# Kernel optimization log

Measured on AMD Instinct MI355X. Metric: run time of the kernel, lower is better.

Reference implementation:

```python
import jax, jax.numpy as jnp
import numpy as np

H = 16  # n_heads


def setup_inputs() -> dict:
    key = jax.random.key(0)
    ks = jax.random.split(key, 8)
    N, L, dm = 4, 2048, 1024
    scale = 0.02
    rn = lambda k, shape: jax.random.normal(k, shape, dtype=jnp.float32)
    return {
        "queries": rn(ks[0], (N, L, dm)),
        "keys": rn(ks[1], (N, L, dm)),
        "values": rn(ks[2], (N, L, dm)),
        "Wq": rn(ks[3], (dm, dm)) * scale, "bq": jnp.zeros((dm,), jnp.float32),
        "Wk": rn(ks[4], (dm, dm)) * scale, "bk": jnp.zeros((dm,), jnp.float32),
        "Wv": rn(ks[5], (dm, dm)) * scale, "bv": jnp.zeros((dm,), jnp.float32),
        "Wo": rn(ks[6], (dm, dm)) * scale, "bo": jnp.zeros((dm,), jnp.float32),
    }


def _forward(queries, keys, values, Wq, bq, Wk, bk, Wv, bv, Wo, bo):
    N, L, _ = queries.shape
    q = (queries @ Wq + bq).reshape(N, L, H, -1)  # [N,L,H,D]
    k = (keys @ Wk + bk).reshape(N, L, H, -1)     # [N,L,H,D]
    v = (values @ Wv + bv).reshape(N, L, H, -1)   # [N,L,H,K]
    qp = jax.nn.elu(q) + 1.0
    kp = jax.nn.elu(k) + 1.0
    D = qp.shape[-1]
    K = v.shape[-1]

    # Causal linear attention: cumulative outer-product recurrence over time.
    def step(sums, inp):
        q_t, k_t, v_t = inp  # each [N,H,D] / [N,H,K]
        sums = sums + jnp.einsum('bhd,bhk->bhdk', k_t, v_t)
        out_t = jnp.einsum('bhdk,bhd->bhk', sums, q_t)
        return sums, out_t

    init = jnp.zeros((N, H, D, K), qp.dtype)
    xs = (jnp.swapaxes(qp, 0, 1), jnp.swapaxes(kp, 0, 1), jnp.swapaxes(v, 0, 1))
    _, res = jax.lax.scan(step, init, xs)  # [L,N,H,K]
    res = jnp.swapaxes(res, 0, 1)          # [N,L,H,K]
    # Original divides elementwise by cumsum of query features (D == K).
    Z = jnp.cumsum(qp, axis=1)             # [N,L,H,D]
    out = (res / Z).reshape(N, L, -1)
    return out @ Wo + bo


def reference(queries, keys, values, Wq, bq, Wk, bk, Wv, bv, Wo, bo):
    return _forward(queries, keys, values, Wq, bq, Wk, bk, Wv, bv, Wo, bo)
```

## Files before the change

kernel.cpp:

```cpp
#include <hip/hip_runtime.h>
#include <hip/hip_bf16.h>

typedef __hip_bfloat16 bf16;

#define N_B   4
#define LSEQ  2048
#define DM    1024
#define NH    16
#define HD    64
#define MROWS (N_B * LSEQ)
#define TCH   64
#define NC    (LSEQ / TCH)
#define PS    72

typedef short bf16x8 __attribute__((ext_vector_type(8)));
typedef float f32x4  __attribute__((ext_vector_type(4)));

__device__ __forceinline__ float u2f(unsigned short u){ return __uint_as_float(((unsigned)u) << 16); }
__device__ __forceinline__ unsigned short f2u(float x){
    bf16 h = __float2bfloat16(x);
    return *reinterpret_cast<unsigned short*>(&h);
}

__device__ __forceinline__ void g2l16(const void* g, void* l) {
    __builtin_amdgcn_global_load_lds(
        (const __attribute__((address_space(1))) unsigned int*)g,
        (__attribute__((address_space(3))) unsigned int*)l, 16, 0, 0);
}

__global__ __launch_bounds__(256) void cvt3_f32_bf16(
    const float* __restrict__ x0, const float* __restrict__ x1, const float* __restrict__ x2,
    bf16* __restrict__ y0, bf16* __restrict__ y1, bf16* __restrict__ y2, int per)
{
    int which = blockIdx.x / per;
    const float* x = (which == 0) ? x0 : (which == 1) ? x1 : x2;
    bf16* y = (which == 0) ? y0 : (which == 1) ? y1 : y2;
    int i = (blockIdx.x - which * per) * 256 + threadIdx.x;
    float4 v = ((const float4*)x)[i];
    ushort4 o = make_ushort4(f2u(v.x), f2u(v.y), f2u(v.z), f2u(v.w));
    ((ushort4*)y)[i] = o;
}

__global__ __launch_bounds__(256) void transpose_w4(
    const float* __restrict__ W0, const float* __restrict__ W1,
    const float* __restrict__ W2, const float* __restrict__ W3,
    bf16* __restrict__ T0, bf16* __restrict__ T1,
    bf16* __restrict__ T2, bf16* __restrict__ T3)
{
    const int z = blockIdx.z;
    const float* W = (z == 0) ? W0 : (z == 1) ? W1 : (z == 2) ? W2 : W3;
    bf16* Wt = (z == 0) ? T0 : (z == 1) ? T1 : (z == 2) ? T2 : T3;

    __shared__ unsigned short t[64][65];
    const int n0 = blockIdx.x * 64;
    const int k0 = blockIdx.y * 64;
    #pragma unroll
    for (int i = 0; i < 16; ++i) {
        int e = i * 256 + threadIdx.x;
        int r = e >> 6, c = e & 63;
        t[c][r] = f2u(W[(size_t)(k0 + r) * DM + n0 + c]);
    }
    __syncthreads();
    #pragma unroll
    for (int i = 0; i < 16; ++i) {
        int e = i * 256 + threadIdx.x;
        int r = e >> 6, c = e & 63;
        ((unsigned short*)Wt)[(size_t)(n0 + r) * DM + k0 + c] = t[r][c];
    }
}

template <typename TO>
__global__ __launch_bounds__(256) void gemm_mfma3(
    const bf16* __restrict__ A0, const bf16* __restrict__ A1, const bf16* __restrict__ A2,
    const bf16* __restrict__ B0, const bf16* __restrict__ B1, const bf16* __restrict__ B2,
    const float* __restrict__ c0, const float* __restrict__ c1, const float* __restrict__ c2,
    TO* __restrict__ C0, TO* __restrict__ C1, TO* __restrict__ C2,
    int actMask, int M, int N, int K)
{
    const int z = blockIdx.z;
    const bf16* A  = (z == 0) ? A0 : (z == 1) ? A1 : A2;
    const bf16* Bt = (z == 0) ? B0 : (z == 1) ? B1 : B2;
    const float* bias = (z == 0) ? c0 : (z == 1) ? c1 : c2;
    TO* C = (z == 0) ? C0 : (z == 1) ? C1 : C2;
    const int act = (actMask >> z) & 1;

    __shared__ __align__(16) short As[128 * 32];
    __shared__ __align__(16) short Bs[128 * 32];

    const int tid  = threadIdx.x;
    const int m0   = blockIdx.x * 128;
    const int n0   = blockIdx.y * 128;
    const int wave = tid >> 6;
    const int lane = tid & 63;
    const int wm   = (wave >> 1) * 64;
    const int wn   = (wave & 1) * 64;
    const int quad = lane >> 4;
    const int l16  = lane & 15;
    const int ksw  = (quad ^ (l16 & 3)) * 8;

    f32x4 acc[4][4] = {};

    for (int k0i = 0; k0i < K; k0i += 32) {
        #pragma unroll
        for (int i = 0; i < 2; ++i) {
            int e = i * 256 + tid;
            int row = e >> 2, kg = e & 3;
            int kgs = (kg ^ (row & 3)) * 8;
            g2l16(A  + (size_t)(m0 + row) * K + k0i + kgs, As + e * 8);
            g2l16(Bt + (size_t)(n0 + row) * K + k0i + kgs, Bs + e * 8);
        }
        __syncthreads();

        bf16x8 af[4], bf_[4];
        #pragma unroll
        for (int mi = 0; mi < 4; ++mi)
            af[mi] = *(const bf16x8*)&As[(wm + mi * 16 + l16) * 32 + ksw];
        #pragma unroll
        for (int ni = 0; ni < 4; ++ni)
            bf_[ni] = *(const bf16x8*)&Bs[(wn + ni * 16 + l16) * 32 + ksw];

        #pragma unroll
        for (int mi = 0; mi < 4; ++mi)
            #pragma unroll
            for (int ni = 0; ni < 4; ++ni)
                acc[mi][ni] = __builtin_amdgcn_mfma_f32_16x16x32_bf16(
                    af[mi], bf_[ni], acc[mi][ni], 0, 0, 0);

        __syncthreads();
    }

    #pragma unroll
    for (int ni = 0; ni < 4; ++ni) {
        int col = n0 + wn + ni * 16 + l16;
        float bv = bias[col];
        #pragma unroll
        for (int mi = 0; mi < 4; ++mi) {
            #pragma unroll
            for (int r = 0; r < 4; ++r) {
                int row = m0 + wm + mi * 16 + quad * 4 + r;
                float x = acc[mi][ni][r] + bv;
                if (act) x = (x > 0.f) ? (x + 1.f) : __expf(x);
                if constexpr (sizeof(TO) == 2)
                    ((bf16*)C)[(size_t)row * N + col] = __float2bfloat16(x);
                else
                    ((float*)C)[(size_t)row * N + col] = x;
            }
        }
    }
}

__global__ __launch_bounds__(256) void chunk_state(
    const bf16* __restrict__ qp, const bf16* __restrict__ kp,
    const bf16* __restrict__ v,
    bf16* __restrict__ chunkSB, float* __restrict__ chunkZ)
{
    __shared__ __align__(16) unsigned short kpT_s[64 * PS];
    __shared__ __align__(16) unsigned short vT_s [64 * PS];
    __shared__ __align__(16) unsigned short qp_s [64 * PS];
    __shared__ float red[4][64];

    const int bh = blockIdx.x;
    const int c  = blockIdx.y;
    const int n  = bh >> 4, h = bh & 15;
    const int tid = threadIdx.x;
    const size_t rowbase = (size_t)n * LSEQ + (size_t)c * TCH;

    #pragma unroll
    for (int r = 0; r < 4; ++r) {
        int q = r * 256 + tid;
        int t = q >> 4, c0 = (q & 15) * 4;
        size_t g = (rowbase + t) * DM + h * HD + c0;
        ushort4 ku = *(const ushort4*)((const unsigned short*)kp + g);
        ushort4 vu = *(const ushort4*)((const unsigned short*)v  + g);
        ushort4 qu = *(const ushort4*)((const unsigned short*)qp + g);
        kpT_s[(c0+0)*PS + t] = ku.x;  kpT_s[(c0+1)*PS + t] = ku.y;
        kpT_s[(c0+2)*PS + t] = ku.z;  kpT_s[(c0+3)*PS + t] = ku.w;
        vT_s [(c0+0)*PS + t] = vu.x;  vT_s [(c0+1)*PS + t] = vu.y;
        vT_s [(c0+2)*PS + t] = vu.z;  vT_s [(c0+3)*PS + t] = vu.w;
        *(ushort4*)&qp_s[t * PS + c0] = qu;
    }
    __syncthreads();

    const int wave = tid >> 6, lane = tid & 63;
    const int quad = lane >> 4, l16 = lane & 15;

    f32x4 acc[4] = {};
    #pragma unroll
    for (int kk = 0; kk < 2; ++kk) {
        bf16x8 af = *(const bf16x8*)&kpT_s[(wave*16 + l16) * PS + kk*32 + quad*8];
        #pragma unroll
        for (int ni = 0; ni < 4; ++ni) {
            bf16x8 bfr = *(const bf16x8*)&vT_s[(ni*16 + l16) * PS + kk*32 + quad*8];
            acc[ni] = __builtin_amdgcn_mfma_f32_16x16x32_bf16(af, bfr, acc[ni], 0, 0, 0);
        }
    }
    unsigned short* Sout = (unsigned short*)chunkSB + (((size_t)bh * NC + c) << 12);
    #pragma unroll
    for (int ni = 0; ni < 4; ++ni) {
        int k = ni*16 + l16;
        #pragma unroll
        for (int r = 0; r < 4; ++r) {
            int d = wave*16 + quad*4 + r;
            Sout[d * 64 + k] = f2u(acc[ni][r]);
        }
    }

    {
        int d = tid & 63, part = tid >> 6;
        float s = 0.f;
        #pragma unroll
        for (int t = part*16; t < part*16 + 16; ++t)
            s += u2f(qp_s[t * PS + d]);
        red[part][d] = s;
    }
    __syncthreads();
    if (tid < 64)
        chunkZ[((size_t)bh * NC + c) * 64 + tid] =
            red[0][tid] + red[1][tid] + red[2][tid] + red[3][tid];
}

__global__ __launch_bounds__(256) void prefix_state(
    const bf16* __restrict__ chunkSB, bf16* __restrict__ SpB,
    float* __restrict__ chunkZ)
{
    const int bh = blockIdx.x;
    const int elem = blockIdx.y * 256 + threadIdx.x;
    const unsigned short* p = (const unsigned short*)chunkSB + (((size_t)bh * NC) << 12) + elem;
    unsigned short* o = (unsigned short*)SpB + (((size_t)bh * NC) << 12) + elem;
    float run = 0.f;
    #pragma unroll
    for (int c = 0; c < NC; ++c) {
        float x = u2f(p[(size_t)c << 12]);
        o[(size_t)c << 12] = f2u(run);
        run += x;
    }
    if (blockIdx.y == 0 && threadIdx.x < 64) {
        float* pz = chunkZ + (size_t)bh * NC * 64 + threadIdx.x;
        float rz = 0.f;
        for (int c = 0; c < NC; ++c) {
            float x = pz[c * 64];
            pz[c * 64] = rz;
            rz += x;
        }
    }
}

__global__ __launch_bounds__(256) void chunk_attn(
    const bf16* __restrict__ qp, const bf16* __restrict__ kp,
    const bf16* __restrict__ v, const bf16* __restrict__ SpB,
    const float* __restrict__ chunkZ, bf16* __restrict__ att)
{
    __shared__ __align__(16) unsigned short qp_s [64 * PS];
    __shared__ __align__(16) unsigned short kp_s [64 * PS];
    __shared__ __align__(16) unsigned short SpT_s[64 * PS];
    __shared__ __align__(16) unsigned short vT_s [64 * PS];
    __shared__ __align__(16) unsigned short qpT_s[64 * PS];
    __shared__ __align__(16) unsigned short P_s  [64 * PS];

    const int bh = blockIdx.x;
    const int c  = blockIdx.y;
    const int n  = bh >> 4, h = bh & 15;
    const int tid = threadIdx.x;
    const size_t rowbase = (size_t)n * LSEQ + (size_t)c * TCH;
    const unsigned short* Spb = (const unsigned short*)SpB + (((size_t)bh * NC + c) << 12);

    #pragma unroll
    for (int r = 0; r < 4; ++r) {
        int q = r * 256 + tid;
        int t = q >> 4, c0 = (q & 15) * 4;
        size_t g = (rowbase + t) * DM + h * HD + c0;
        ushort4 qu = *(const ushort4*)((const unsigned short*)qp + g);
        ushort4 ku = *(const ushort4*)((const unsigned short*)kp + g);
        ushort4 vu = *(const ushort4*)((const unsigned short*)v  + g);
        ushort4 su = *(const ushort4*)(Spb + q * 4);
        *(ushort4*)&qp_s[t * PS + c0] = qu;
        *(ushort4*)&kp_s[t * PS + c0] = ku;
        vT_s [(c0+0)*PS + t] = vu.x;  vT_s [(c0+1)*PS + t] = vu.y;
        vT_s [(c0+2)*PS + t] = vu.z;  vT_s [(c0+3)*PS + t] = vu.w;
        qpT_s[(c0+0)*PS + t] = qu.x;  qpT_s[(c0+1)*PS + t] = qu.y;
        qpT_s[(c0+2)*PS + t] = qu.z;  qpT_s[(c0+3)*PS + t] = qu.w;
        SpT_s[(c0+0)*PS + t] = su.x;  SpT_s[(c0+1)*PS + t] = su.y;
        SpT_s[(c0+2)*PS + t] = su.z;  SpT_s[(c0+3)*PS + t] = su.w;
    }
    __syncthreads();

    const int wave = tid >> 6, lane = tid & 63;
    const int quad = lane >> 4, l16 = lane & 15;
    const int mrow = wave * 16;

    f32x4 acc[4]  = {};
    f32x4 zacc[4] = {};
    f32x4 pacc[4] = {};

    const unsigned short ONE = 0x3F80;

    #pragma unroll
    for (int kk = 0; kk < 2; ++kk) {
        bf16x8 af = *(const bf16x8*)&qp_s[(mrow + l16) * PS + kk*32 + quad*8];
        bf16x8 tf;
        #pragma unroll
        for (int j = 0; j < 8; ++j) {
            int s = kk*32 + quad*8 + j;
            tf[j] = (short)((s <= mrow + l16) ? ONE : 0);
        }
        #pragma unroll
        for (int ni = 0; ni < 4; ++ni) {
            int boff = (ni*16 + l16) * PS + kk*32 + quad*8;
            bf16x8 b_sp = *(const bf16x8*)&SpT_s[boff];
            bf16x8 b_kp = *(const bf16x8*)&kp_s [boff];
            bf16x8 b_qt = *(const bf16x8*)&qpT_s[boff];
            acc [ni] = __builtin_amdgcn_mfma_f32_16x16x32_bf16(af, b_sp, acc [ni], 0, 0, 0);
            pacc[ni] = __builtin_amdgcn_mfma_f32_16x16x32_bf16(af, b_kp, pacc[ni], 0, 0, 0);
            zacc[ni] = __builtin_amdgcn_mfma_f32_16x16x32_bf16(tf, b_qt, zacc[ni], 0, 0, 0);
        }
    }

    #pragma unroll
    for (int ni = 0; ni < 4; ++ni) {
        int s = ni*16 + l16;
        #pragma unroll
        for (int r = 0; r < 4; ++r) {
            int t = mrow + quad*4 + r;
            float pv = (s <= t) ? pacc[ni][r] : 0.f;
            P_s[t * PS + s] = f2u(pv);
        }
    }
    __syncthreads();

    #pragma unroll
    for (int kk = 0; kk < 2; ++kk) {
        bf16x8 af = *(const bf16x8*)&P_s[(mrow + l16) * PS + kk*32 + quad*8];
        #pragma unroll
        for (int ni = 0; ni < 4; ++ni) {
            bf16x8 b_v = *(const bf16x8*)&vT_s[(ni*16 + l16) * PS + kk*32 + quad*8];
            acc[ni] = __builtin_amdgcn_mfma_f32_16x16x32_bf16(af, b_v, acc[ni], 0, 0, 0);
        }
    }

    #pragma unroll
    for (int ni = 0; ni < 4; ++ni) {
        int k = ni*16 + l16;
        float zp = chunkZ[((size_t)bh * NC + c) * 64 + k];
        #pragma unroll
        for (int r = 0; r < 4; ++r) {
            int t = mrow + quad*4 + r;
            float o = acc[ni][r] / (zp + zacc[ni][r]);
            ((unsigned short*)att)[(rowbase + t) * DM + h * HD + k] = f2u(o);
        }
    }
}

extern "C" void kernel_launch(void* const* d_in, const int* in_sizes, int n_in,
                              void* d_out, int out_size, void* d_ws, size_t ws_size,
                              hipStream_t stream)
{
    const float* queries = (const float*)d_in[0];
    const float* keys    = (const float*)d_in[1];
    const float* values  = (const float*)d_in[2];
    const float* Wq = (const float*)d_in[3];
    const float* bq = (const float*)d_in[4];
    const float* Wk = (const float*)d_in[5];
    const float* bk = (const float*)d_in[6];
    const float* Wv = (const float*)d_in[7];
    const float* bv = (const float*)d_in[8];
    const float* Wo = (const float*)d_in[9];
    const float* bo = (const float*)d_in[10];
    float* out = (float*)d_out;

    char* w = (char*)d_ws;
    const size_t E2 = (size_t)MROWS * DM * 2;
    const size_t WB = (size_t)DM * DM * 2;
    bf16* qb  = (bf16*)(w + 0 * E2);
    bf16* kb  = (bf16*)(w + 1 * E2);
    bf16* vb  = (bf16*)(w + 2 * E2);
    bf16* Wqt = (bf16*)(w + 3 * E2 + 0 * WB);
    bf16* Wkt = (bf16*)(w + 3 * E2 + 1 * WB);
    bf16* Wvt = (bf16*)(w + 3 * E2 + 2 * WB);
    bf16* Wot = (bf16*)(w + 3 * E2 + 3 * WB);
    bf16* qp  = (bf16*)(w + 3 * E2 + 4 * WB);
    bf16* kp  = (bf16*)(w + 4 * E2 + 4 * WB);
    bf16* vv  = (bf16*)(w + 5 * E2 + 4 * WB);
    bf16* SpB = (bf16*)(w + 6 * E2 + 4 * WB);
    bf16*  chunkSB = kb;
    float* chunkZ  = (float*)Wqt;
    bf16*  att     = qb;

    const int n4 = (MROWS * DM) / 4;
    const int per = n4 / 256;
    cvt3_f32_bf16<<<3 * per, 256, 0, stream>>>(queries, keys, values, qb, kb, vb, per);

    transpose_w4<<<dim3(DM / 64, DM / 64, 4), 256, 0, stream>>>(
        Wq, Wk, Wv, Wo, Wqt, Wkt, Wvt, Wot);

    gemm_mfma3<bf16><<<dim3(MROWS / 128, DM / 128, 3), 256, 0, stream>>>(
        qb, kb, vb, Wqt, Wkt, Wvt, bq, bk, bv, qp, kp, vv,
        0b011, MROWS, DM, DM);

    chunk_state <<<dim3(64, NC), 256, 0, stream>>>(qp, kp, vv, chunkSB, chunkZ);
    prefix_state<<<dim3(64, 16), 256, 0, stream>>>(chunkSB, SpB, chunkZ);
    chunk_attn  <<<dim3(64, NC), 256, 0, stream>>>(qp, kp, vv, SpB, chunkZ, att);

    gemm_mfma3<float><<<dim3(MROWS / 128, DM / 128, 1), 256, 0, stream>>>(
        att, att, att, Wot, Wot, Wot, bo, bo, bo, out, out, out,
        0, MROWS, DM, DM);
}
```

Measured before the change: 312.0 us.

## Pipeline GEMM global-to-LDS loads with a 4-buffer ring and explicit vmcnt waits

```diff
diff --git a/kernel.cpp b/kernel.cpp
--- a/kernel.cpp
+++ b/kernel.cpp
@@ -70,7 +70,7 @@
 }
 
 template <typename TO>
-__global__ __launch_bounds__(256) void gemm_mfma3(
+__global__ __launch_bounds__(256, 2) void gemm_mfma3(
     const bf16* __restrict__ A0, const bf16* __restrict__ A1, const bf16* __restrict__ A2,
     const bf16* __restrict__ B0, const bf16* __restrict__ B1, const bf16* __restrict__ B2,
     const float* __restrict__ c0, const float* __restrict__ c1, const float* __restrict__ c2,
@@ -84,8 +84,8 @@
     TO* C = (z == 0) ? C0 : (z == 1) ? C1 : C2;
     const int act = (actMask >> z) & 1;
 
-    __shared__ __align__(16) short As[128 * 32];
-    __shared__ __align__(16) short Bs[128 * 32];
+    __shared__ __align__(16) short As[4 * 128 * 32];
+    __shared__ __align__(16) short Bs[4 * 128 * 32];
 
     const int tid  = threadIdx.x;
     const int m0   = blockIdx.x * 128;
@@ -100,33 +100,57 @@
 
     f32x4 acc[4][4] = {};
 
-    for (int k0i = 0; k0i < K; k0i += 32) {
+    const int NT = K >> 5;
+
+    auto stage = [&](int t, int buf) {
+        const int k0i = t << 5;
+        short* Ad = As + buf * (128 * 32);
+        short* Bd = Bs + buf * (128 * 32);
         #pragma unroll
         for (int i = 0; i < 2; ++i) {
             int e = i * 256 + tid;
             int row = e >> 2, kg = e & 3;
             int kgs = (kg ^ (row & 3)) * 8;
-            g2l16(A  + (size_t)(m0 + row) * K + k0i + kgs, As + e * 8);
-            g2l16(Bt + (size_t)(n0 + row) * K + k0i + kgs, Bs + e * 8);
-        }
-        __syncthreads();
-
-        bf16x8 af[4], bf_[4];
+            g2l16(A  + (size_t)(m0 + row) * K + k0i + kgs, Ad + e * 8);
+            g2l16(Bt + (size_t)(n0 + row) * K + k0i + kgs, Bd + e * 8);
+        }
+    };
+
+    auto compute = [&](int buf) {
+        const short* Ab = As + buf * (128 * 32);
+        const short* Bb = Bs + buf * (128 * 32);
+        bf16x8 af[4], bfr[4];
         #pragma unroll
         for (int mi = 0; mi < 4; ++mi)
-            af[mi] = *(const bf16x8*)&As[(wm + mi * 16 + l16) * 32 + ksw];
+            af[mi] = *(const bf16x8*)&Ab[(wm + mi * 16 + l16) * 32 + ksw];
         #pragma unroll
         for (int ni = 0; ni < 4; ++ni)
-            bf_[ni] = *(const bf16x8*)&Bs[(wn + ni * 16 + l16) * 32 + ksw];
-
+            bfr[ni] = *(const bf16x8*)&Bb[(wn + ni * 16 + l16) * 32 + ksw];
+        __builtin_amdgcn_s_setprio(1);
         #pragma unroll
         for (int mi = 0; mi < 4; ++mi)
             #pragma unroll
             for (int ni = 0; ni < 4; ++ni)
                 acc[mi][ni] = __builtin_amdgcn_mfma_f32_16x16x32_bf16(
-                    af[mi], bf_[ni], acc[mi][ni], 0, 0, 0);
-
-        __syncthreads();
+                    af[mi], bfr[ni], acc[mi][ni], 0, 0, 0);
+        __builtin_amdgcn_s_setprio(0);
+    };
+
+    stage(0, 0);
+    stage(1, 1);
+    stage(2, 2);
+
+    for (int t = 0; t < NT; ++t) {
+        if (t < NT - 2)
+            asm volatile("s_waitcnt vmcnt(8)" ::: "memory");
+        else if (t == NT - 2)
+            asm volatile("s_waitcnt vmcnt(4)" ::: "memory");
+        else
+            asm volatile("s_waitcnt vmcnt(0)" ::: "memory");
+        __builtin_amdgcn_s_barrier();
+        __builtin_amdgcn_sched_barrier(0);
+        if (t + 3 < NT) stage(t + 3, (t + 3) & 3);
+        compute(t & 3);
     }
 
     #pragma unroll
```

After: 316.9 us. No clear change (+1.6%).

## Rewrite GEMM as 256x256 tile, 8-wave, double-buffered pipelined MFMA kernel

Applied to the files above, without the earlier changes.

```diff
diff --git a/kernel.cpp b/kernel.cpp
--- a/kernel.cpp
+++ b/kernel.cpp
@@ -70,7 +70,7 @@
 }
 
 template <typename TO>
-__global__ __launch_bounds__(256) void gemm_mfma3(
+__global__ __launch_bounds__(512, 2) void gemm_mfma3(
     const bf16* __restrict__ A0, const bf16* __restrict__ A1, const bf16* __restrict__ A2,
     const bf16* __restrict__ B0, const bf16* __restrict__ B1, const bf16* __restrict__ B2,
     const float* __restrict__ c0, const float* __restrict__ c1, const float* __restrict__ c2,
@@ -84,60 +84,164 @@
     TO* C = (z == 0) ? C0 : (z == 1) ? C1 : C2;
     const int act = (actMask >> z) & 1;
 
-    __shared__ __align__(16) short As[128 * 32];
-    __shared__ __align__(16) short Bs[128 * 32];
+    __shared__ __align__(16) short smem[2 * 2 * 2 * 128 * 64];
 
     const int tid  = threadIdx.x;
-    const int m0   = blockIdx.x * 128;
-    const int n0   = blockIdx.y * 128;
+    const int m0   = blockIdx.x * 256;
+    const int n0   = blockIdx.y * 256;
     const int wave = tid >> 6;
     const int lane = tid & 63;
-    const int wm   = (wave >> 1) * 64;
-    const int wn   = (wave & 1) * 64;
+    const int wm   = wave >> 2;
+    const int wn   = wave & 3;
     const int quad = lane >> 4;
     const int l16  = lane & 15;
-    const int ksw  = (quad ^ (l16 & 3)) * 8;
-
-    f32x4 acc[4][4] = {};
-
-    for (int k0i = 0; k0i < K; k0i += 32) {
+    const int xsw  = l16 & 7;
+
+    f32x4 acc[8][4] = {};
+    bf16x8 Areg[4][2], Breg[4][2];
+
+    const int NT = K >> 6;
+
+    auto stageA = [&](int t, int half, int buf) {
+        short* dst = smem + (((buf << 2) | 0 | half) << 13);
         #pragma unroll
         for (int i = 0; i < 2; ++i) {
-            int e = i * 256 + tid;
-            int row = e >> 2, kg = e & 3;
-            int kgs = (kg ^ (row & 3)) * 8;
-            g2l16(A  + (size_t)(m0 + row) * K + k0i + kgs, As + e * 8);
-            g2l16(Bt + (size_t)(n0 + row) * K + k0i + kgs, Bs + e * 8);
-        }
-        __syncthreads();
-
-        bf16x8 af[4], bf_[4];
-        #pragma unroll
-        for (int mi = 0; mi < 4; ++mi)
-            af[mi] = *(const bf16x8*)&As[(wm + mi * 16 + l16) * 32 + ksw];
-        #pragma unroll
-        for (int ni = 0; ni < 4; ++ni)
-            bf_[ni] = *(const bf16x8*)&Bs[(wn + ni * 16 + l16) * 32 + ksw];
-
-        #pragma unroll
-        for (int mi = 0; mi < 4; ++mi)
+            int e = i * 512 + tid;
+            int r = e >> 3;
+            int col = ((e & 7) ^ (r & 7)) * 8;
+            int grow = m0 + half * 64 + (r & 63) + ((r >> 6) << 7);
+            g2l16(A + (size_t)grow * K + t * 64 + col, dst + e * 8);
+        }
+    };
+    auto stageB = [&](int t, int half, int buf) {
+        short* dst = smem + (((buf << 2) | 2 | half) << 13);
+        #pragma unroll
+        for (int i = 0; i < 2; ++i) {
+            int e = i * 512 + tid;
+            int r = e >> 3;
+            int col = ((e & 7) ^ (r & 7)) * 8;
+            int grow = n0 + ((r >> 5) << 6) + half * 32 + (r & 31);
+            g2l16(Bt + (size_t)grow * K + t * 64 + col, dst + e * 8);
+        }
+    };
+
+    auto ldA = [&](const short* base, int m2, int ks) -> bf16x8 {
+        int row  = wm * 64 + m2 * 16 + l16;
+        int slot = (ks * 4 + quad) ^ xsw;
+        return *(const bf16x8*)(base + row * 64 + slot * 8);
+    };
+    auto ldB = [&](const short* base, int n2, int ks) -> bf16x8 {
+        int row  = wn * 32 + n2 * 16 + l16;
+        int slot = (ks * 4 + quad) ^ xsw;
+        return *(const bf16x8*)(base + row * 64 + slot * 8);
+    };
+
+    stageA(0, 0, 0); stageB(0, 0, 0); stageB(0, 1, 0); stageA(0, 1, 0);
+    stageA(1, 0, 1); stageB(1, 0, 1);
+    asm volatile("s_waitcnt vmcnt(4)" ::: "memory");
+    asm volatile("s_barrier" ::: "memory");
+
+    for (int T = 0; T < NT; ++T) {
+        const int bT = T & 1;
+        const short* Ab0 = smem + (((bT << 2) | 0 | 0) << 13);
+        const short* Ab1 = smem + (((bT << 2) | 0 | 1) << 13);
+        const short* Bb0 = smem + (((bT << 2) | 2 | 0) << 13);
+        const short* Bb1 = smem + (((bT << 2) | 2 | 1) << 13);
+
+        #pragma unroll
+        for (int m2 = 0; m2 < 4; ++m2) {
+            Areg[m2][0] = ldA(Ab0, m2, 0);
+            Areg[m2][1] = ldA(Ab0, m2, 1);
+        }
+        #pragma unroll
+        for (int n2 = 0; n2 < 2; ++n2) {
+            Breg[n2][0] = ldB(Bb0, n2, 0);
+            Breg[n2][1] = ldB(Bb0, n2, 1);
+        }
+        if (T + 1 < NT) stageB(T + 1, 1, (T + 1) & 1);
+        asm volatile("s_barrier" ::: "memory");
+        __builtin_amdgcn_s_setprio(1);
+        #pragma unroll
+        for (int m2 = 0; m2 < 4; ++m2)
             #pragma unroll
-            for (int ni = 0; ni < 4; ++ni)
-                acc[mi][ni] = __builtin_amdgcn_mfma_f32_16x16x32_bf16(
-                    af[mi], bf_[ni], acc[mi][ni], 0, 0, 0);
-
-        __syncthreads();
+            for (int n2 = 0; n2 < 2; ++n2) {
+                acc[m2][n2] = __builtin_amdgcn_mfma_f32_16x16x32_bf16(
+                    Areg[m2][0], Breg[n2][0], acc[m2][n2], 0, 0, 0);
+                acc[m2][n2] = __builtin_amdgcn_mfma_f32_16x16x32_bf16(
+                    Areg[m2][1], Breg[n2][1], acc[m2][n2], 0, 0, 0);
+            }
+        __builtin_amdgcn_s_setprio(0);
+        asm volatile("s_barrier" ::: "memory");
+
+        #pragma unroll
+        for (int n2 = 0; n2 < 2; ++n2) {
+            Breg[2 + n2][0] = ldB(Bb1, n2, 0);
+            Breg[2 + n2][1] = ldB(Bb1, n2, 1);
+        }
+        if (T + 1 < NT) stageA(T + 1, 1, (T + 1) & 1);
+        asm volatile("s_barrier" ::: "memory");
+        __builtin_amdgcn_s_setprio(1);
+        #pragma unroll
+        for (int m2 = 0; m2 < 4; ++m2)
+            #pragma unroll
+            for (int n2 = 0; n2 < 2; ++n2) {
+                acc[m2][2 + n2] = __builtin_amdgcn_mfma_f32_16x16x32_bf16(
+                    Areg[m2][0], Breg[2 + n2][0], acc[m2][2 + n2], 0, 0, 0);
+                acc[m2][2 + n2] = __builtin_amdgcn_mfma_f32_16x16x32_bf16(
+                    Areg[m2][1], Breg[2 + n2][1], acc[m2][2 + n2], 0, 0, 0);
+            }
+        __builtin_amdgcn_s_setprio(0);
+        asm volatile("s_barrier" ::: "memory");
+
+        #pragma unroll
+        for (int m2 = 0; m2 < 4; ++m2) {
+            Areg[m2][0] = ldA(Ab1, m2, 0);
+            Areg[m2][1] = ldA(Ab1, m2, 1);
+        }
+        if (T + 2 < NT) stageA(T + 2, 0, bT);
+        asm volatile("s_barrier" ::: "memory");
+        __builtin_amdgcn_s_setprio(1);
+        #pragma unroll
+        for (int m2 = 0; m2 < 4; ++m2)
+            #pragma unroll
+            for (int n2 = 0; n2 < 2; ++n2) {
+                acc[4 + m2][n2] = __builtin_amdgcn_mfma_f32_16x16x32_bf16(
+                    Areg[m2][0], Breg[n2][0], acc[4 + m2][n2], 0, 0, 0);
+                acc[4 + m2][n2] = __builtin_amdgcn_mfma_f32_16x16x32_bf16(
+                    Areg[m2][1], Breg[n2][1], acc[4 + m2][n2], 0, 0, 0);
+            }
+        __builtin_amdgcn_s_setprio(0);
+        asm volatile("s_barrier" ::: "memory");
+
+        if (T + 2 < NT) stageB(T + 2, 0, bT);
+        asm volatile("s_barrier" ::: "memory");
+        __builtin_amdgcn_s_setprio(1);
+        #pragma unroll
+        for (int m2 = 0; m2 < 4; ++m2)
+            #pragma unroll
+            for (int n2 = 0; n2 < 2; ++n2) {
+                acc[4 + m2][2 + n2] = __builtin_amdgcn_mfma_f32_16x16x32_bf16(
+                    Areg[m2][0], Breg[2 + n2][0], acc[4 + m2][2 + n2], 0, 0, 0);
+                acc[4 + m2][2 + n2] = __builtin_amdgcn_mfma_f32_16x16x32_bf16(
+                    Areg[m2][1], Breg[2 + n2][1], acc[4 + m2][2 + n2], 0, 0, 0);
+            }
+        __builtin_amdgcn_s_setprio(0);
+        if (T < NT - 2)
+            asm volatile("s_waitcnt vmcnt(4)" ::: "memory");
+        else
+            asm volatile("s_waitcnt vmcnt(0)" ::: "memory");
+        asm volatile("s_barrier" ::: "memory");
     }
 
     #pragma unroll
     for (int ni = 0; ni < 4; ++ni) {
-        int col = n0 + wn + ni * 16 + l16;
+        int col = n0 + wn * 64 + ni * 16 + l16;
         float bv = bias[col];
         #pragma unroll
-        for (int mi = 0; mi < 4; ++mi) {
+        for (int mi = 0; mi < 8; ++mi) {
             #pragma unroll
             for (int r = 0; r < 4; ++r) {
-                int row = m0 + wm + mi * 16 + quad * 4 + r;
+                int row = m0 + wm * 128 + mi * 16 + quad * 4 + r;
                 float x = acc[mi][ni][r] + bv;
                 if (act) x = (x > 0.f) ? (x + 1.f) : __expf(x);
                 if constexpr (sizeof(TO) == 2)
@@ -392,7 +496,7 @@
     transpose_w4<<<dim3(DM / 64, DM / 64, 4), 256, 0, stream>>>(
         Wq, Wk, Wv, Wo, Wqt, Wkt, Wvt, Wot);
 
-    gemm_mfma3<bf16><<<dim3(MROWS / 128, DM / 128, 3), 256, 0, stream>>>(
+    gemm_mfma3<bf16><<<dim3(MROWS / 256, DM / 256, 3), 512, 0, stream>>>(
         qb, kb, vb, Wqt, Wkt, Wvt, bq, bk, bv, qp, kp, vv,
         0b011, MROWS, DM, DM);
 
@@ -400,7 +504,7 @@
     prefix_state<<<dim3(64, 16), 256, 0, stream>>>(chunkSB, SpB, chunkZ);
     chunk_attn  <<<dim3(64, NC), 256, 0, stream>>>(qp, kp, vv, SpB, chunkZ, att);
 
-    gemm_mfma3<float><<<dim3(MROWS / 128, DM / 128, 1), 256, 0, stream>>>(
+    gemm_mfma3<float><<<dim3(MROWS / 256, DM / 256, 1), 512, 0, stream>>>(
         att, att, att, Wot, Wot, Wot, bo, bo, bo, out, out, out,
         0, MROWS, DM, DM);
 }
```

Measured after the change: 313.6 us. No clear change (+0.5%).
